# Kernel tuning notes

Measured on AMD Instinct MI355X. Metric: run time of the kernel, lower is better.

The kernel has to match this reference:

```python
import jax, jax.numpy as jnp
import numpy as np

EMBED_DIM = 1024
NUM_HEADS = 16
HEAD_DIM = EMBED_DIM // NUM_HEADS


def setup_inputs() -> dict:
    key = jax.random.key(0)
    ks = jax.random.split(key, 9)
    B, T, D = 2, 4096, EMBED_DIM
    scale = 1.0 / np.sqrt(D)
    x = jax.random.normal(ks[0], (B, T, D), dtype=jnp.float32)
    # nn.Linear weights stored as (out, in); we use (in, out) layout via transpose-free init
    Wq = jax.random.uniform(ks[1], (D, D), dtype=jnp.float32, minval=-scale, maxval=scale)
    Wk = jax.random.uniform(ks[2], (D, D), dtype=jnp.float32, minval=-scale, maxval=scale)
    Wv = jax.random.uniform(ks[3], (D, D), dtype=jnp.float32, minval=-scale, maxval=scale)
    Wo = jax.random.uniform(ks[4], (D, D), dtype=jnp.float32, minval=-scale, maxval=scale)
    bq = jax.random.uniform(ks[5], (D,), dtype=jnp.float32, minval=-scale, maxval=scale)
    bk = jax.random.uniform(ks[6], (D,), dtype=jnp.float32, minval=-scale, maxval=scale)
    bv = jax.random.uniform(ks[7], (D,), dtype=jnp.float32, minval=-scale, maxval=scale)
    bo = jax.random.uniform(ks[8], (D,), dtype=jnp.float32, minval=-scale, maxval=scale)
    return {"x": x, "Wq": Wq, "bq": bq, "Wk": Wk, "bk": bk,
            "Wv": Wv, "bv": bv, "Wo": Wo, "bo": bo}


def reference(x, Wq, bq, Wk, bk, Wv, bv, Wo, bo):
    B, T, D = x.shape
    H, Hd = NUM_HEADS, HEAD_DIM
    q = x @ Wq + bq  # [B,T,D]
    k = x @ Wk + bk
    v = x @ Wv + bv
    # [B,T,D] -> [B,H,T,Hd]
    q = q.reshape(B, T, H, Hd).transpose(0, 2, 1, 3)
    k = k.reshape(B, T, H, Hd).transpose(0, 2, 1, 3)
    v = v.reshape(B, T, H, Hd).transpose(0, 2, 1, 3)
    att = jnp.einsum('bhqd,bhkd->bhqk', q, k) / jnp.sqrt(jnp.float32(Hd))
    causal = jnp.tril(jnp.ones((T, T), dtype=bool))  # True = keep
    att = jnp.where(causal, att, -jnp.inf)
    att = jax.nn.softmax(att, axis=-1)
    out = jnp.einsum('bhqk,bhkd->bhqd', att, v)  # [B,H,T,Hd]
    out = out.transpose(0, 2, 1, 3).reshape(B, T, D)
    return out @ Wo + bo
```

## Files before the change

kernel.cpp:

```cpp
#include <hip/hip_runtime.h>
#include <hip/hip_bf16.h>
#include <math.h>

typedef __bf16 bf16;
typedef __attribute__((ext_vector_type(8))) __bf16 bf16x8;
typedef __attribute__((ext_vector_type(4))) __bf16 bf16x4;
typedef __attribute__((ext_vector_type(4))) short short4v;
typedef __attribute__((ext_vector_type(4))) float f32x4;

#define MFMA16(a,b,c)  __builtin_amdgcn_mfma_f32_16x16x32_bf16((a),(b),(c),0,0,0)
#define MFMAK16(a,b,c) __builtin_amdgcn_mfma_f32_16x16x16bf16_1k((a),(b),(c),0,0,0)

__device__ __forceinline__ void gload16(const void* gp, void* lp) {
  __builtin_amdgcn_global_load_lds(
      (const __attribute__((address_space(1))) void*)gp,
      (__attribute__((address_space(3))) void*)lp, 16, 0, 0);
}

__global__ __launch_bounds__(256) void cast_x(
    const float* __restrict__ x, bf16* __restrict__ xb)
{
  size_t i = ((size_t)blockIdx.x*256 + threadIdx.x) * 8;
  f32x4 a = *(const f32x4*)(x+i);
  f32x4 b = *(const f32x4*)(x+i+4);
  bf16x8 o;
  #pragma unroll
  for (int j=0;j<4;j++) { o[j] = (bf16)a[j]; o[4+j] = (bf16)b[j]; }
  *(bf16x8*)(xb+i) = o;
}

__global__ __launch_bounds__(1024) void tr_cast(
    const float* __restrict__ w0, const float* __restrict__ w1,
    const float* __restrict__ w2, bf16* __restrict__ dst)
{
  __shared__ bf16 tile[64][65];
  const float* src = (blockIdx.z==0)?w0:(blockIdx.z==1)?w1:w2;
  bf16* d = dst + (size_t)blockIdx.z * (1024*1024);
  int x = threadIdx.x, y = threadIdx.y;
  int tc = blockIdx.x, tr = blockIdx.y;
  #pragma unroll
  for (int i=0;i<4;i++) {
    int r = y + i*16;
    tile[r][x] = (bf16)src[(size_t)(tr*64+r)*1024 + tc*64 + x];
  }
  __syncthreads();
  #pragma unroll
  for (int i=0;i<4;i++) {
    int r = y + i*16;
    d[(size_t)(tc*64+r)*1024 + tr*64 + x] = tile[x][r];
  }
}

__global__ __launch_bounds__(1024) void v_tr(
    const bf16* __restrict__ v, bf16* __restrict__ vt)
{
  __shared__ bf16 tile[64][65];
  int x = threadIdx.x, y = threadIdx.y;
  int tt = blockIdx.x;
  int bh = blockIdx.y;
  int b = bh >> 4, h = bh & 15;
  const bf16* src = v + ((size_t)b*4096 + tt*64)*1024 + h*64;
  bf16* dst = vt + ((size_t)bh*64)*4096 + tt*64;
  #pragma unroll
  for (int i=0;i<4;i++) {
    int r = y + i*16;
    tile[r][x] = src[(size_t)r*1024 + x];
  }
  __syncthreads();
  #pragma unroll
  for (int i=0;i<4;i++) {
    int r = y + i*16;
    dst[(size_t)r*4096 + x] = tile[x][r];
  }
}

__global__ __launch_bounds__(256) void gemm_qkv(
    const bf16* __restrict__ A, const bf16* __restrict__ Bt,
    const float* __restrict__ bq, const float* __restrict__ bk, const float* __restrict__ bv,
    bf16* __restrict__ q, bf16* __restrict__ k, bf16* __restrict__ v,
    int M, int K)
{
  __shared__ __align__(16) bf16 As[128*32];
  __shared__ __align__(16) bf16 Bs[128*32];
  const int tid  = threadIdx.x;
  const int wave = tid >> 6;
  const int lane = tid & 63;
  const int l15  = lane & 15;
  const int quad = lane >> 4;
  const int m0 = blockIdx.y * 128;
  const int n0 = blockIdx.x * 128;
  const int wm = (wave >> 1) * 64;
  const int wn = (wave & 1) * 64;
  const int srow = lane >> 2;
  const int scol = (lane & 3) * 8;

  f32x4 acc[4][4];
  #pragma unroll
  for (int i=0;i<4;i++)
    #pragma unroll
    for (int j=0;j<4;j++)
      acc[i][j] = (f32x4){0.f,0.f,0.f,0.f};

  for (int k0 = 0; k0 < K; k0 += 32) {
    __syncthreads();
    #pragma unroll
    for (int p=0;p<2;p++) {
      int c = p*4 + wave;
      int row = c*16 + srow;
      gload16(A  + (size_t)(m0+row)*K + k0 + scol, As + c*512);
      gload16(Bt + (size_t)(n0+row)*K + k0 + scol, Bs + c*512);
    }
    __syncthreads();
    bf16x8 af[4], bfr[4];
    #pragma unroll
    for (int t=0;t<4;t++) {
      af[t]  = *(const bf16x8*)(As + (wm + t*16 + l15)*32 + quad*8);
      bfr[t] = *(const bf16x8*)(Bs + (wn + t*16 + l15)*32 + quad*8);
    }
    #pragma unroll
    for (int mt=0;mt<4;mt++)
      #pragma unroll
      for (int nt=0;nt<4;nt++)
        acc[mt][nt] = MFMA16(af[mt], bfr[nt], acc[mt][nt]);
  }

  const int mat = n0 >> 10;
  const float* bsel = (mat==0) ? bq : (mat==1) ? bk : bv;
  bf16*       osel  = (mat==0) ? q  : (mat==1) ? k  : v;
  const float qsc   = (mat==0) ? 0.1803368801f : 1.0f;
  #pragma unroll
  for (int nt=0;nt<4;nt++) {
    int col = n0 + wn + nt*16 + l15;
    int cw  = col & 1023;
    float bvv = bsel[cw];
    #pragma unroll
    for (int mt=0;mt<4;mt++) {
      int row = m0 + wm + mt*16 + quad*4;
      #pragma unroll
      for (int r=0;r<4;r++)
        osel[(size_t)(row + r)*1024 + cw] = (bf16)((acc[mt][nt][r] + bvv) * qsc);
    }
  }
}

__global__ __launch_bounds__(256) void gemm_out(
    const bf16* __restrict__ A, const bf16* __restrict__ Bt,
    const float* __restrict__ bias, float* __restrict__ C,
    int M, int N, int K)
{
  __shared__ __align__(16) bf16 As[128*32];
  __shared__ __align__(16) bf16 Bs[128*32];
  const int tid  = threadIdx.x;
  const int wave = tid >> 6;
  const int lane = tid & 63;
  const int l15  = lane & 15;
  const int quad = lane >> 4;
  const int m0 = blockIdx.y * 128;
  const int n0 = blockIdx.x * 128;
  const int wm = (wave >> 1) * 64;
  const int wn = (wave & 1) * 64;
  const int srow = lane >> 2;
  const int scol = (lane & 3) * 8;

  f32x4 acc[4][4];
  #pragma unroll
  for (int i=0;i<4;i++)
    #pragma unroll
    for (int j=0;j<4;j++)
      acc[i][j] = (f32x4){0.f,0.f,0.f,0.f};

  for (int k0 = 0; k0 < K; k0 += 32) {
    __syncthreads();
    #pragma unroll
    for (int p=0;p<2;p++) {
      int c = p*4 + wave;
      int row = c*16 + srow;
      gload16(A  + (size_t)(m0+row)*K + k0 + scol, As + c*512);
      gload16(Bt + (size_t)(n0+row)*K + k0 + scol, Bs + c*512);
    }
    __syncthreads();
    bf16x8 af[4], bfr[4];
    #pragma unroll
    for (int t=0;t<4;t++) {
      af[t]  = *(const bf16x8*)(As + (wm + t*16 + l15)*32 + quad*8);
      bfr[t] = *(const bf16x8*)(Bs + (wn + t*16 + l15)*32 + quad*8);
    }
    #pragma unroll
    for (int mt=0;mt<4;mt++)
      #pragma unroll
      for (int nt=0;nt<4;nt++)
        acc[mt][nt] = MFMA16(af[mt], bfr[nt], acc[mt][nt]);
  }

  #pragma unroll
  for (int nt=0;nt<4;nt++) {
    int col = n0 + wn + nt*16 + l15;
    float bvv = bias[col];
    #pragma unroll
    for (int mt=0;mt<4;mt++) {
      int row = m0 + wm + mt*16 + quad*4;
      #pragma unroll
      for (int r=0;r<4;r++)
        C[(size_t)(row + r)*N + col] = acc[mt][nt][r] + bvv;
    }
  }
}

__global__ __launch_bounds__(256, 4) void attn_fwd(
    const bf16* __restrict__ Q, const bf16* __restrict__ Kp,
    const bf16* __restrict__ Vtg, bf16* __restrict__ O)
{
  __shared__ __align__(16) char KsB[2*8192];
  __shared__ __align__(16) char VtB[2*8192];

  const int tid  = threadIdx.x;
  const int w    = tid >> 6;
  const int lane = tid & 63;
  const int l15  = lane & 15;
  const int quad = lane >> 4;

  const int bid = blockIdx.x;
  const int pp  = bid >> 5;
  const int bh  = bid & 31;
  const int h   = bh & 15;
  const int b   = bh >> 4;

  const size_t headoff = (size_t)h * 64;
  const size_t bbase   = (size_t)b * 4096;

  short4v ones_s;
  {
    bf16x4 o1;
    #pragma unroll
    for (int j=0;j<4;j++) o1[j] = (bf16)1.0f;
    ones_s = __builtin_bit_cast(short4v, o1);
  }

  const int kt_row = tid >> 2;
  const int kswz   = (kt_row & 7) << 4;
  const int ks_w0  = kt_row*128 + (((tid & 3)*32)      ^ kswz);
  const int ks_w1  = kt_row*128 + (((tid & 3)*32 + 16) ^ kswz);

  const int vd  = tid >> 2;
  const int vt0 = (tid & 3) * 16;
  int vw[4];
  #pragma unroll
  for (int u=0;u<4;u++)
    vw[u] = vd*128 + (((vt0 + u*4)*2) ^ ((vd & 15) << 3));

  const int s7    = l15 & 7;
  const int ks_r0 = l15*128 + ((quad ^ (s7 & 3)) << 4) + ((s7 >> 2) << 6);
  const int ks_r1 = ks_r0 ^ 64;
  const int vt_rbase = l15*128 + ((quad ^ (l15 & 3)) << 3) + ((l15 >> 2) << 5);
  int vt_r[4];
  #pragma unroll
  for (int tt=0;tt<4;tt++) vt_r[tt] = vt_rbase ^ (tt << 5);

  const bf16* kbase0 = Kp  + (bbase + kt_row)*1024 + headoff + (tid & 3)*16;
  const bf16* vbase0 = Vtg + ((size_t)(bh*64) + vd)*4096 + vt0;

  for (int ph = 0; ph < 2; ++ph) {
    const int qt = ph ? (63 - pp) : pp;
    const int q0 = qt * 64;

    bf16x8 aq[2];
    {
      int row = q0 + w*16 + l15;
      const bf16* qp = Q + (bbase + row)*1024 + headoff + quad*8;
      aq[0] = *(const bf16x8*)(qp);
      aq[1] = *(const bf16x8*)(qp + 32);
    }

    f32x4 acco[4];
    f32x4 accli;
    #pragma unroll
    for (int i=0;i<4;i++) acco[i] = (f32x4){0.f,0.f,0.f,0.f};
    accli = (f32x4){0.f,0.f,0.f,0.f};

    __syncthreads();
    {
      bf16x8 k0 = *(const bf16x8*)(kbase0);
      bf16x8 k1 = *(const bf16x8*)(kbase0 + 8);
      *(bf16x8*)(KsB + ks_w0) = k0;
      *(bf16x8*)(KsB + ks_w1) = k1;
      bf16x8 v0 = *(const bf16x8*)(vbase0);
      bf16x8 v1 = *(const bf16x8*)(vbase0 + 8);
      *(bf16x4*)(VtB + vw[0]) = __builtin_shufflevector(v0, v0, 0,1,2,3);
      *(bf16x4*)(VtB + vw[1]) = __builtin_shufflevector(v0, v0, 4,5,6,7);
      *(bf16x4*)(VtB + vw[2]) = __builtin_shufflevector(v1, v1, 0,1,2,3);
      *(bf16x4*)(VtB + vw[3]) = __builtin_shufflevector(v1, v1, 4,5,6,7);
    }
    __syncthreads();

    const bf16* kpref = kbase0 + 64*1024;
    const bf16* vpref = vbase0 + 64;

    for (int kt = 0; kt <= qt; ++kt) {
      const int p = kt & 1;
      const bool pre = (kt < qt);

      bf16x8 kr0, kr1, vr0, vr1;
      if (pre) {
        kr0 = *(const bf16x8*)(kpref);
        kr1 = *(const bf16x8*)(kpref + 8);
        vr0 = *(const bf16x8*)(vpref);
        vr1 = *(const bf16x8*)(vpref + 8);
        kpref += 64*1024;
        vpref += 64;
      }

      const char* ksb = KsB + p*8192;
      const char* vtb = VtB + p*8192;

      f32x4 accs[4];
      #pragma unroll
      for (int i=0;i<4;i++) accs[i] = (f32x4){0.f,0.f,0.f,0.f};

      __builtin_amdgcn_s_setprio(1);
      #pragma unroll
      for (int kk=0;kk<2;kk++) {
        #pragma unroll
        for (int tt=0;tt<4;tt++) {
          bf16x8 ka = *(const bf16x8*)(ksb + (kk ? ks_r1 : ks_r0) + tt*2048);
          accs[tt] = MFMA16(ka, aq[kk], accs[tt]);
        }
      }
      __builtin_amdgcn_s_setprio(0);

      short4v pts[4];
      if (kt == qt) {
        #pragma unroll
        for (int tt=0;tt<4;tt++) {
          bf16x4 pb;
          #pragma unroll
          for (int r=0;r<4;r++) {
            float pf = __builtin_amdgcn_exp2f(fminf(accs[tt][r], 60.0f));
            if (tt*16 + quad*4 + r > w*16 + l15) pf = 0.0f;
            pb[r] = (bf16)pf;
          }
          pts[tt] = __builtin_bit_cast(short4v, pb);
        }
      } else {
        #pragma unroll
        for (int tt=0;tt<4;tt++) {
          bf16x4 pb;
          #pragma unroll
          for (int r=0;r<4;r++)
            pb[r] = (bf16)__builtin_amdgcn_exp2f(fminf(accs[tt][r], 60.0f));
          pts[tt] = __builtin_bit_cast(short4v, pb);
        }
      }

      __builtin_amdgcn_s_setprio(1);
      #pragma unroll
      for (int nt=0;nt<4;nt++) {
        #pragma unroll
        for (int tt=0;tt<4;tt++) {
          bf16x4 va = *(const bf16x4*)(vtb + vt_r[tt] + nt*2048);
          acco[nt] = MFMAK16(__builtin_bit_cast(short4v, va), pts[tt], acco[nt]);
        }
      }
      #pragma unroll
      for (int tt=0;tt<4;tt++)
        accli = MFMAK16(ones_s, pts[tt], accli);
      __builtin_amdgcn_s_setprio(0);

      if (pre) {
        char* ksn = KsB + (p^1)*8192;
        char* vtn = VtB + (p^1)*8192;
        *(bf16x8*)(ksn + ks_w0) = kr0;
        *(bf16x8*)(ksn + ks_w1) = kr1;
        *(bf16x4*)(vtn + vw[0]) = __builtin_shufflevector(vr0, vr0, 0,1,2,3);
        *(bf16x4*)(vtn + vw[1]) = __builtin_shufflevector(vr0, vr0, 4,5,6,7);
        *(bf16x4*)(vtn + vw[2]) = __builtin_shufflevector(vr1, vr1, 0,1,2,3);
        *(bf16x4*)(vtn + vw[3]) = __builtin_shufflevector(vr1, vr1, 4,5,6,7);
        __syncthreads();
      }
    }

    {
      float inv = 1.0f / accli[0];
      int qrow = q0 + w*16 + l15;
      bf16* ob = O + (bbase + qrow)*1024 + headoff;
      #pragma unroll
      for (int nt=0;nt<4;nt++) {
        bf16x4 o;
        #pragma unroll
        for (int r=0;r<4;r++) o[r] = (bf16)(acco[nt][r] * inv);
        *(bf16x4*)(ob + nt*16 + quad*4) = o;
      }
    }
  }
}

extern "C" void kernel_launch(void* const* d_in, const int* in_sizes, int n_in,
                              void* d_out, int out_size, void* d_ws, size_t ws_size,
                              hipStream_t stream) {
  const float* x  = (const float*)d_in[0];
  const float* Wq = (const float*)d_in[1];
  const float* bq = (const float*)d_in[2];
  const float* Wk = (const float*)d_in[3];
  const float* bk = (const float*)d_in[4];
  const float* Wv = (const float*)d_in[5];
  const float* bv = (const float*)d_in[6];
  const float* Wo = (const float*)d_in[7];
  const float* bo = (const float*)d_in[8];
  float* out = (float*)d_out;

  bf16* ws = (bf16*)d_ws;
  bf16* q  = ws;
  bf16* k  = q + (size_t)8192*1024;
  bf16* v  = k + (size_t)8192*1024;
  bf16* xb = v + (size_t)8192*1024;
  bf16* ao = q;
  bf16* WtQKV = (bf16*)d_out;
  bf16* vT    = (bf16*)d_out;
  bf16* WtO   = xb;

  tr_cast<<<dim3(16,16,3), dim3(64,16), 0, stream>>>(Wq, Wk, Wv, WtQKV);
  cast_x<<<4096, 256, 0, stream>>>(x, xb);
  gemm_qkv<<<dim3(24,64), 256, 0, stream>>>(xb, WtQKV, bq, bk, bv, q, k, v, 8192, 1024);
  v_tr<<<dim3(64,32), dim3(64,16), 0, stream>>>(v, vT);
  tr_cast<<<dim3(16,16,1), dim3(64,16), 0, stream>>>(Wo, Wo, Wo, WtO);
  attn_fwd<<<1024, 256, 0, stream>>>(q, k, vT, ao);
  gemm_out<<<dim3(8,64), 256, 0, stream>>>(ao, WtO, bo, out, 8192, 1024, 1024);
}
```

Baseline: 329.2 us.

## Process two 64-row query tiles per attention block to reuse staged K/V

Each attention workgroup now handles a 128-row query tile as two 64-row sub-tiles, A and B. Every K and V tile staged in LDS feeds MFMAs for both, so the K/V global loads and LDS staging are amortised over twice the work. The causal masking is split so that A masks the diagonal tile and B masks the following one. In exchange the grid is halved, launch bounds drop to two blocks per CU, and register pressure roughly doubles for the accumulators, which reduces occupancy and latency hiding.

```diff
diff --git a/kernel.cpp b/kernel.cpp
--- a/kernel.cpp
+++ b/kernel.cpp
@@ -206,7 +206,7 @@
   }
 }
 
-__global__ __launch_bounds__(256, 4) void attn_fwd(
+__global__ __launch_bounds__(256, 2) void attn_fwd(
     const bf16* __restrict__ Q, const bf16* __restrict__ Kp,
     const bf16* __restrict__ Vtg, bf16* __restrict__ O)
 {
@@ -260,22 +260,26 @@
   const bf16* vbase0 = Vtg + ((size_t)(bh*64) + vd)*4096 + vt0;
 
   for (int ph = 0; ph < 2; ++ph) {
-    const int qt = ph ? (63 - pp) : pp;
-    const int q0 = qt * 64;
-
-    bf16x8 aq[2];
+    const int qt = ph ? (31 - pp) : pp;
+    const int q0 = qt * 128;
+    const int ktmax = 2*qt + 1;
+
+    bf16x8 aqA[2], aqB[2];
     {
-      int row = q0 + w*16 + l15;
-      const bf16* qp = Q + (bbase + row)*1024 + headoff + quad*8;
-      aq[0] = *(const bf16x8*)(qp);
-      aq[1] = *(const bf16x8*)(qp + 32);
-    }
-
-    f32x4 acco[4];
-    f32x4 accli;
-    #pragma unroll
-    for (int i=0;i<4;i++) acco[i] = (f32x4){0.f,0.f,0.f,0.f};
-    accli = (f32x4){0.f,0.f,0.f,0.f};
+      int rowA = q0 + w*16 + l15;
+      const bf16* qp = Q + (bbase + rowA)*1024 + headoff + quad*8;
+      aqA[0] = *(const bf16x8*)(qp);
+      aqA[1] = *(const bf16x8*)(qp + 32);
+      qp += 64*1024;
+      aqB[0] = *(const bf16x8*)(qp);
+      aqB[1] = *(const bf16x8*)(qp + 32);
+    }
+
+    f32x4 accoA[4], accoB[4], accliA, accliB;
+    #pragma unroll
+    for (int i=0;i<4;i++) { accoA[i] = (f32x4){0.f,0.f,0.f,0.f}; accoB[i] = (f32x4){0.f,0.f,0.f,0.f}; }
+    accliA = (f32x4){0.f,0.f,0.f,0.f};
+    accliB = (f32x4){0.f,0.f,0.f,0.f};
 
     __syncthreads();
     {
@@ -295,9 +299,9 @@
     const bf16* kpref = kbase0 + 64*1024;
     const bf16* vpref = vbase0 + 64;
 
-    for (int kt = 0; kt <= qt; ++kt) {
+    for (int kt = 0; kt <= ktmax; ++kt) {
       const int p = kt & 1;
-      const bool pre = (kt < qt);
+      const bool pre = (kt < ktmax);
 
       bf16x8 kr0, kr1, vr0, vr1;
       if (pre) {
@@ -312,9 +316,9 @@
       const char* ksb = KsB + p*8192;
       const char* vtb = VtB + p*8192;
 
-      f32x4 accs[4];
-      #pragma unroll
-      for (int i=0;i<4;i++) accs[i] = (f32x4){0.f,0.f,0.f,0.f};
+      f32x4 accsA[4], accsB[4];
+      #pragma unroll
+      for (int i=0;i<4;i++) { accsA[i] = (f32x4){0.f,0.f,0.f,0.f}; accsB[i] = (f32x4){0.f,0.f,0.f,0.f}; }
 
       __builtin_amdgcn_s_setprio(1);
       #pragma unroll
@@ -322,32 +326,41 @@
         #pragma unroll
         for (int tt=0;tt<4;tt++) {
           bf16x8 ka = *(const bf16x8*)(ksb + (kk ? ks_r1 : ks_r0) + tt*2048);
-          accs[tt] = MFMA16(ka, aq[kk], accs[tt]);
+          accsA[tt] = MFMA16(ka, aqA[kk], accsA[tt]);
+          accsB[tt] = MFMA16(ka, aqB[kk], accsB[tt]);
         }
       }
       __builtin_amdgcn_s_setprio(0);
 
-      short4v pts[4];
-      if (kt == qt) {
+      short4v ptsA[4], ptsB[4];
+      if (kt < 2*qt) {
         #pragma unroll
         for (int tt=0;tt<4;tt++) {
-          bf16x4 pb;
+          bf16x4 pa, pb;
           #pragma unroll
           for (int r=0;r<4;r++) {
-            float pf = __builtin_amdgcn_exp2f(fminf(accs[tt][r], 60.0f));
-            if (tt*16 + quad*4 + r > w*16 + l15) pf = 0.0f;
-            pb[r] = (bf16)pf;
+            pa[r] = (bf16)__builtin_amdgcn_exp2f(fminf(accsA[tt][r], 60.0f));
+            pb[r] = (bf16)__builtin_amdgcn_exp2f(fminf(accsB[tt][r], 60.0f));
           }
-          pts[tt] = __builtin_bit_cast(short4v, pb);
+          ptsA[tt] = __builtin_bit_cast(short4v, pa);
+          ptsB[tt] = __builtin_bit_cast(short4v, pb);
         }
       } else {
+        const bool adead = (kt > 2*qt);
         #pragma unroll
         for (int tt=0;tt<4;tt++) {
-          bf16x4 pb;
+          bf16x4 pa, pb;
           #pragma unroll
-          for (int r=0;r<4;r++)
-            pb[r] = (bf16)__builtin_amdgcn_exp2f(fminf(accs[tt][r], 60.0f));
-          pts[tt] = __builtin_bit_cast(short4v, pb);
+          for (int r=0;r<4;r++) {
+            const bool tq = (tt*16 + quad*4 + r > w*16 + l15);
+            float fa = __builtin_amdgcn_exp2f(fminf(accsA[tt][r], 60.0f));
+            if (adead || tq) fa = 0.0f;
+            float fb = __builtin_amdgcn_exp2f(fminf(accsB[tt][r], 60.0f));
+            if (adead && tq) fb = 0.0f;
+            pa[r] = (bf16)fa; pb[r] = (bf16)fb;
+          }
+          ptsA[tt] = __builtin_bit_cast(short4v, pa);
+          ptsB[tt] = __builtin_bit_cast(short4v, pb);
         }
       }
 
@@ -357,12 +370,16 @@
         #pragma unroll
         for (int tt=0;tt<4;tt++) {
           bf16x4 va = *(const bf16x4*)(vtb + vt_r[tt] + nt*2048);
-          acco[nt] = MFMAK16(__builtin_bit_cast(short4v, va), pts[tt], acco[nt]);
+          short4v vas = __builtin_bit_cast(short4v, va);
+          accoA[nt] = MFMAK16(vas, ptsA[tt], accoA[nt]);
+          accoB[nt] = MFMAK16(vas, ptsB[tt], accoB[nt]);
         }
       }
       #pragma unroll
-      for (int tt=0;tt<4;tt++)
-        accli = MFMAK16(ones_s, pts[tt], accli);
+      for (int tt=0;tt<4;tt++) {
+        accliA = MFMAK16(ones_s, ptsA[tt], accliA);
+        accliB = MFMAK16(ones_s, ptsB[tt], accliB);
+      }
       __builtin_amdgcn_s_setprio(0);
 
       if (pre) {
@@ -379,15 +396,21 @@
     }
 
     {
-      float inv = 1.0f / accli[0];
-      int qrow = q0 + w*16 + l15;
-      bf16* ob = O + (bbase + qrow)*1024 + headoff;
+      float invA = 1.0f / accliA[0];
+      float invB = 1.0f / accliB[0];
+      int rowA = q0 + w*16 + l15;
+      bf16* obA = O + (bbase + rowA)*1024 + headoff;
+      bf16* obB = obA + 64*1024;
       #pragma unroll
       for (int nt=0;nt<4;nt++) {
-        bf16x4 o;
+        bf16x4 oA, oB;
         #pragma unroll
-        for (int r=0;r<4;r++) o[r] = (bf16)(acco[nt][r] * inv);
-        *(bf16x4*)(ob + nt*16 + quad*4) = o;
+        for (int r=0;r<4;r++) {
+          oA[r] = (bf16)(accoA[nt][r] * invA);
+          oB[r] = (bf16)(accoB[nt][r] * invB);
+        }
+        *(bf16x4*)(obA + nt*16 + quad*4) = oA;
+        *(bf16x4*)(obB + nt*16 + quad*4) = oB;
       }
     }
   }
@@ -422,6 +445,6 @@
   gemm_qkv<<<dim3(24,64), 256, 0, stream>>>(xb, WtQKV, bq, bk, bv, q, k, v, 8192, 1024);
   v_tr<<<dim3(64,32), dim3(64,16), 0, stream>>>(v, vT);
   tr_cast<<<dim3(16,16,1), dim3(64,16), 0, stream>>>(Wo, Wo, Wo, WtO);
-  attn_fwd<<<1024, 256, 0, stream>>>(q, k, vT, ao);
+  attn_fwd<<<512, 256, 0, stream>>>(q, k, vT, ao);
   gemm_out<<<dim3(8,64), 256, 0, stream>>>(ao, WtO, bo, out, 8192, 1024, 1024);
 }
```

Measured after the change: 325.5 us. Within noise of the previous version (-1.2%).
